# Performance work log

Hardware: AMD Instinct MI355X
Metric: run time of the kernel (lower is better)

Reference implementation:

```python
import jax, jax.numpy as jnp
import numpy as np

SIG = 0.5        # varifold Gaussian kernel bandwidth on edge centers
SRNF_W = 1e-7    # weight of SRNF/SRVF regularizer (matches 1e-07 in source)
LEN_EPS = 1e-12  # guard against zero-length edges


def _edge_data(V, E):
    # V: [N, D] vertices, E: [M, 2] int edge list
    v0 = V[E[:, 0]]
    v1 = V[E[:, 1]]
    c = 0.5 * (v0 + v1)                                  # edge centers [M, D]
    t = v1 - v0                                          # tangent vectors [M, D]
    l = jnp.sqrt(jnp.sum(t * t, axis=-1) + LEN_EPS)      # edge lengths [M]
    u = t / l[:, None]                                   # unit tangents [M, D]
    return c, l, u


def _vari_inner(a, b):
    # oriented-varifold scalar product <mu_a, mu_b> with Gaussian spatial kernel
    # and squared-cosine tangent kernel, weighted by edge lengths
    cX, lX, uX = a
    cY, lY, uY = b
    d2 = jnp.sum((cX[:, None, :] - cY[None, :, :]) ** 2, axis=-1)  # [Mx, My]
    K = jnp.exp(-d2 / (SIG * SIG))
    ang = (uX @ uY.T) ** 2                                         # [Mx, My]
    return jnp.sum(K * ang * (lX[:, None] * lY[None, :]))


def _srvf(V, E):
    # square-root velocity field per edge: q = sqrt(|t|) * t/|t|
    _, l, u = _edge_data(V, E)
    return u * jnp.sqrt(l)[:, None]


def _per_sample(out_i, tgt_i, tedges_i, template, edges):
    X = out_i + template
    a = _edge_data(X, edges)
    b = _edge_data(tgt_i, tedges_i)
    # varifold distance^2 between deformed template and target curve
    vari = _vari_inner(a, a) - 2.0 * _vari_inner(a, b) + _vari_inner(b, b)
    # SRNF shape regularizer to the template
    q_diff = _srvf(X, edges) - _srvf(template, edges)
    return vari + SRNF_W * jnp.sum(q_diff ** 2)


def setup_inputs() -> dict:
    key = jax.random.key(0)
    k1, k2, k3 = jax.random.split(key, 3)
    B, N, D = 8, 2000, 3
    E = N - 1
    edges = jnp.stack([jnp.arange(E), jnp.arange(E) + 1], axis=1).astype(jnp.int32)
    tedges = jnp.broadcast_to(edges[None], (B, E, 2))
    template = jax.random.normal(k1, (N, D), dtype=jnp.float32) * 0.5
    output = jax.random.normal(k2, (B, N, D), dtype=jnp.float32) * 0.1
    target = jax.random.normal(k3, (B, N, D), dtype=jnp.float32) * 0.5
    return {"output": output, "target": target, "tedges": tedges,
            "template": template, "edges": edges}


def reference(output, target, tedges, template, edges):
    # vectorized over the original Python batch loop
    losses = jax.vmap(lambda o, t, te: _per_sample(o, t, te, template, edges))(
        output, target, tedges)
    return jnp.mean(losses)
```

## Files before the change

### kernel.cpp

```cpp
#include <hip/hip_runtime.h>
#include <math.h>

#define E_CNT 1999
#define N_PTS 2000
#define B_CNT 8
#define SEG 2048
#define NTILES 16
#define NTP 136
#define TOTAL_BLOCKS (B_CNT*NTP)

#define HCEXP (-2.8853900817779268f)
#define SQRT_NEG2C 3.3972871f

typedef __attribute__((ext_vector_type(8))) _Float16 half8;
typedef __attribute__((ext_vector_type(4))) float f32x4;
typedef __attribute__((ext_vector_type(4))) int i32x4;

__device__ __forceinline__ half8 mk_frag(int lo, int hi) {
    i32x4 t; t[0] = lo; t[1] = hi; t[2] = 0; t[3] = 0;
    return __builtin_bit_cast(half8, t);
}

__device__ __forceinline__ float edge_rec(
    const float* __restrict__ outp, const float* __restrict__ tgtp,
    const float* __restrict__ tmpl, int b, int slot, bool diagResp,
    i32x4& rec)
{
    float val = 0.f;
    bool isX = (slot < SEG);
    int e = isX ? slot : slot - SEG;
    if (e < E_CNT) {
        float ax, ay, az, bx, by, bz;
        if (isX) {
            const float* o0 = outp + ((size_t)b * N_PTS + e) * 3;
            const float* t0 = tmpl + (size_t)e * 3;
            ax = o0[0] + t0[0]; ay = o0[1] + t0[1]; az = o0[2] + t0[2];
            bx = o0[3] + t0[3]; by = o0[4] + t0[4]; bz = o0[5] + t0[5];
        } else {
            const float* g0 = tgtp + ((size_t)b * N_PTS + e) * 3;
            ax = g0[0]; ay = g0[1]; az = g0[2];
            bx = g0[3]; by = g0[4]; bz = g0[5];
        }
        float cx = 0.5f * (ax + bx), cy = 0.5f * (ay + by), cz = 0.5f * (az + bz);
        float tx = bx - ax, ty = by - ay, tz = bz - az;
        float l2 = tx * tx + ty * ty + tz * tz + 1e-12f;
        float l  = sqrtf(l2);
        float rs = rsqrtf(l);
        float f  = __builtin_amdgcn_exp2f(HCEXP * (cx * cx + cy * cy + cz * cz));
        float g  = rs * f;
        half8 hv;
        hv[0] = (_Float16)(SQRT_NEG2C * cx);
        hv[1] = (_Float16)(SQRT_NEG2C * cy);
        hv[2] = (_Float16)(SQRT_NEG2C * cz);
        hv[3] = (_Float16)0.f;
        hv[4] = (_Float16)(tx * g);
        hv[5] = (_Float16)(ty * g);
        hv[6] = (_Float16)(tz * g);
        hv[7] = (_Float16)0.f;
        rec = __builtin_bit_cast(i32x4, hv);
        if (diagResp) {
            float a0 = (float)hv[0], a1 = (float)hv[1], a2 = (float)hv[2];
            float d0 = (float)hv[4], d1 = (float)hv[5], d2 = (float)hv[6];
            float sarg = a0 * a0 + a1 * a1 + a2 * a2;
            float sdu  = d0 * d0 + d1 * d1 + d2 * d2;
            float self = __builtin_amdgcn_exp2f(sarg) * sdu * sdu;
            val = l * l - self;
            if (isX) {
                const float* t0 = tmpl + (size_t)e * 3;
                float txT = t0[3] - t0[0], tyT = t0[4] - t0[1], tzT = t0[5] - t0[2];
                float lT = sqrtf(txT * txT + tyT * tyT + tzT * tzT + 1e-12f);
                float rT = rsqrtf(lT);
                float dqx = tx * rs - txT * rT;
                float dqy = ty * rs - tyT * rT;
                float dqz = tz * rs - tzT * rT;
                val += 1e-7f * (dqx * dqx + dqy * dqy + dqz * dqz);
            }
        }
    } else {
        i32x4 z; z[0] = 0; z[1] = 0; z[2] = 0; z[3] = 0;
        rec = z;
    }
    return val;
}

__global__ __launch_bounds__(512) void fused_kernel(
    const float* __restrict__ outp, const float* __restrict__ tgtp,
    const float* __restrict__ tmpl, float* __restrict__ part)
{
    __shared__ i32x4 sRec[513];
    __shared__ float red[8];

    int id = blockIdx.x;
    int b  = id / NTP;
    int t  = id % NTP;
    int rt = 0, rem = t;
    while (rem >= NTILES - rt) { rem -= NTILES - rt; ++rt; }
    int ct = rt + rem;

    int tid = threadIdx.x, lane = tid & 63, w = tid >> 6;
    bool isDiag = (rt == ct);

    float dval = 0.f;
    if (tid < 256) {
        i32x4 rrec;
        dval = edge_rec(outp, tgtp, tmpl, b, rt * 256 + tid, isDiag, rrec);
        sRec[tid] = rrec;
    } else {
        int c = tid - 256;
        i32x4 crec;
        edge_rec(outp, tgtp, tmpl, b, ct * 256 + c, false, crec);
        sRec[256 + c] = crec;
    }
    if (tid == 0) {
        i32x4 z; z[0] = 0; z[1] = 0; z[2] = 0; z[3] = 0;
        sRec[512] = z;
    }
    __syncthreads();

    int l15 = lane & 15;
    bool g0 = (lane < 16);

    half8 aArg[2], aDu[2];
    #pragma unroll
    for (int q = 0; q < 2; ++q) {
        i32x4 ra = sRec[g0 ? ((w * 2 + q) * 16 + l15) : 512];
        aArg[q] = mk_frag(ra[0], ra[1]);
        aDu[q]  = mk_frag(ra[2], ra[3]);
    }

    f32x4 av = {0.f, 0.f, 0.f, 0.f};
    #pragma unroll 4
    for (int ctile = 0; ctile < 16; ++ctile) {
        i32x4 rb = sRec[g0 ? (256 + ctile * 16 + l15) : 512];
        half8 bArg = mk_frag(rb[0], rb[1]);
        half8 bDu  = mk_frag(rb[2], rb[3]);
        #pragma unroll
        for (int q = 0; q < 2; ++q) {
            f32x4 zz = {0.f, 0.f, 0.f, 0.f};
            f32x4 dA = __builtin_amdgcn_mfma_f32_16x16x32_f16(aArg[q], bArg, zz, 0, 0, 0);
            f32x4 dD = __builtin_amdgcn_mfma_f32_16x16x32_f16(aDu[q],  bDu,  zz, 0, 0, 0);
            #pragma unroll
            for (int rr = 0; rr < 4; ++rr)
                av[rr] = fmaf(__builtin_amdgcn_exp2f(dA[rr]), dD[rr] * dD[rr], av[rr]);
        }
    }

    float sgn = isDiag ? 1.f : (((rt < 8) == (ct < 8)) ? 2.f : -2.f);
    float thr = fmaf(sgn, (av[0] + av[1]) + (av[2] + av[3]), dval);
    for (int off = 32; off; off >>= 1) thr += __shfl_down(thr, off);
    if (lane == 0) red[w] = thr;
    __syncthreads();
    if (tid == 0) {
        float s = ((red[0] + red[1]) + (red[2] + red[3]))
                + ((red[4] + red[5]) + (red[6] + red[7]));
        part[id] = s;
    }
}

__global__ __launch_bounds__(256) void final_kernel(
    const float* __restrict__ part, float* __restrict__ outv)
{
    float s = 0.f;
    for (int i = threadIdx.x; i < TOTAL_BLOCKS; i += 256) s += part[i];
    for (int off = 32; off; off >>= 1) s += __shfl_down(s, off);
    __shared__ float red[4];
    int lane = threadIdx.x & 63, wid = threadIdx.x >> 6;
    if (lane == 0) red[wid] = s;
    __syncthreads();
    if (threadIdx.x == 0)
        outv[0] = 0.125f * ((red[0] + red[1]) + (red[2] + red[3]));
}

extern "C" void kernel_launch(void* const* d_in, const int* in_sizes, int n_in,
                              void* d_out, int out_size, void* d_ws, size_t ws_size,
                              hipStream_t stream)
{
    const float* outp = (const float*)d_in[0];
    const float* tgtp = (const float*)d_in[1];
    const float* tmpl = (const float*)d_in[3];
    float* part = (float*)d_ws;

    fused_kernel<<<TOTAL_BLOCKS, 512, 0, stream>>>(outp, tgtp, tmpl, part);
    final_kernel<<<1, 256, 0, stream>>>(part, (float*)d_out);
}
```

Baseline: 23.45 us.

## Double block size to one row tile per wave and software-pipeline MFMA loop

Raises the block to 1024 threads so each of 16 waves handles a single 16-row tile instead of two, and restructures the column loop so the MFMA for the next tile is issued before the exp2/accumulate of the current one. The aim is more wave-level parallelism for latency hiding and overlap of matrix-core work with transcendental VALU work. In exchange, per-thread edge preprocessing runs in only half of the threads, the block-level reduction grows to 16 partials, and larger blocks can lower how many blocks fit per CU.

```diff
diff --git a/kernel.cpp b/kernel.cpp
--- a/kernel.cpp
+++ b/kernel.cpp
@@ -83,12 +83,12 @@
     return val;
 }
 
-__global__ __launch_bounds__(512) void fused_kernel(
+__global__ __launch_bounds__(1024) void fused_kernel(
     const float* __restrict__ outp, const float* __restrict__ tgtp,
     const float* __restrict__ tmpl, float* __restrict__ part)
 {
     __shared__ i32x4 sRec[513];
-    __shared__ float red[8];
+    __shared__ float red[16];
 
     int id = blockIdx.x;
     int b  = id / NTP;
@@ -105,13 +105,12 @@
         i32x4 rrec;
         dval = edge_rec(outp, tgtp, tmpl, b, rt * 256 + tid, isDiag, rrec);
         sRec[tid] = rrec;
-    } else {
+    } else if (tid < 512) {
         int c = tid - 256;
         i32x4 crec;
         edge_rec(outp, tgtp, tmpl, b, ct * 256 + c, false, crec);
         sRec[256 + c] = crec;
-    }
-    if (tid == 0) {
+    } else if (tid == 512) {
         i32x4 z; z[0] = 0; z[1] = 0; z[2] = 0; z[3] = 0;
         sRec[512] = z;
     }
@@ -120,29 +119,33 @@
     int l15 = lane & 15;
     bool g0 = (lane < 16);
 
-    half8 aArg[2], aDu[2];
-    #pragma unroll
-    for (int q = 0; q < 2; ++q) {
-        i32x4 ra = sRec[g0 ? ((w * 2 + q) * 16 + l15) : 512];
-        aArg[q] = mk_frag(ra[0], ra[1]);
-        aDu[q]  = mk_frag(ra[2], ra[3]);
+    half8 aArg, aDu;
+    {
+        i32x4 ra = sRec[g0 ? (w * 16 + l15) : 512];
+        aArg = mk_frag(ra[0], ra[1]);
+        aDu  = mk_frag(ra[2], ra[3]);
     }
 
+    const f32x4 zz = {0.f, 0.f, 0.f, 0.f};
     f32x4 av = {0.f, 0.f, 0.f, 0.f};
-    #pragma unroll 4
+
+    f32x4 dA, dD;
+    {
+        i32x4 rb = sRec[g0 ? (256 + l15) : 512];
+        dA = __builtin_amdgcn_mfma_f32_16x16x32_f16(aArg, mk_frag(rb[0], rb[1]), zz, 0, 0, 0);
+        dD = __builtin_amdgcn_mfma_f32_16x16x32_f16(aDu,  mk_frag(rb[2], rb[3]), zz, 0, 0, 0);
+    }
+    #pragma unroll
     for (int ctile = 0; ctile < 16; ++ctile) {
-        i32x4 rb = sRec[g0 ? (256 + ctile * 16 + l15) : 512];
-        half8 bArg = mk_frag(rb[0], rb[1]);
-        half8 bDu  = mk_frag(rb[2], rb[3]);
+        f32x4 cA = dA, cD = dD;
+        if (ctile < 15) {
+            i32x4 rb = sRec[g0 ? (256 + (ctile + 1) * 16 + l15) : 512];
+            dA = __builtin_amdgcn_mfma_f32_16x16x32_f16(aArg, mk_frag(rb[0], rb[1]), zz, 0, 0, 0);
+            dD = __builtin_amdgcn_mfma_f32_16x16x32_f16(aDu,  mk_frag(rb[2], rb[3]), zz, 0, 0, 0);
+        }
         #pragma unroll
-        for (int q = 0; q < 2; ++q) {
-            f32x4 zz = {0.f, 0.f, 0.f, 0.f};
-            f32x4 dA = __builtin_amdgcn_mfma_f32_16x16x32_f16(aArg[q], bArg, zz, 0, 0, 0);
-            f32x4 dD = __builtin_amdgcn_mfma_f32_16x16x32_f16(aDu[q],  bDu,  zz, 0, 0, 0);
-            #pragma unroll
-            for (int rr = 0; rr < 4; ++rr)
-                av[rr] = fmaf(__builtin_amdgcn_exp2f(dA[rr]), dD[rr] * dD[rr], av[rr]);
-        }
+        for (int rr = 0; rr < 4; ++rr)
+            av[rr] = fmaf(__builtin_amdgcn_exp2f(cA[rr]), cD[rr] * cD[rr], av[rr]);
     }
 
     float sgn = isDiag ? 1.f : (((rt < 8) == (ct < 8)) ? 2.f : -2.f);
@@ -151,8 +154,9 @@
     if (lane == 0) red[w] = thr;
     __syncthreads();
     if (tid == 0) {
-        float s = ((red[0] + red[1]) + (red[2] + red[3]))
-                + ((red[4] + red[5]) + (red[6] + red[7]));
+        float s = 0.f;
+        #pragma unroll
+        for (int i = 0; i < 16; ++i) s += red[i];
         part[id] = s;
     }
 }
@@ -180,6 +184,6 @@
     const float* tmpl = (const float*)d_in[3];
     float* part = (float*)d_ws;
 
-    fused_kernel<<<TOTAL_BLOCKS, 512, 0, stream>>>(outp, tgtp, tmpl, part);
+    fused_kernel<<<TOTAL_BLOCKS, 1024, 0, stream>>>(outp, tgtp, tmpl, part);
     final_kernel<<<1, 256, 0, stream>>>(part, (float*)d_out);
 }
```

Result: slower. 26.16 us (+11.5%).
